# Kernel tuning notes

Measured on AMD Instinct MI355X. Metric: run time of the kernel, lower is better.

## Reference

```python
import jax, jax.numpy as jnp
import numpy as np

B, CIN, HALF, H, W = 4, 3, 32, 512, 512
K_MODE, PAD_MODE, N_LEVELS = 11, 5, 17  # 11x11 mode window, reflect pad 5, round(x*255/16) in 0..16
SLOPE, EPS = 0.01, 1e-5


def _leaky(x):
    return jnp.where(x > 0, x, SLOPE * x)


def _bn(x, g, b):
    # BatchNorm2d in training mode: batch statistics over (B,H,W), biased var
    m = x.mean(axis=(0, 2, 3), keepdims=True)
    v = x.var(axis=(0, 2, 3), keepdims=True)
    return (x - m) * jax.lax.rsqrt(v + EPS) * g[None, :, None, None] + b[None, :, None, None]


def _mode_pool(x):
    # quantize to 17 discrete levels, then sliding-window histogram mode (fused
    # equivalent of unfold + torch.mode; argmax first-hit == smallest tied value)
    k = jnp.clip(jnp.round(x * (255.0 / 16.0)), 0, N_LEVELS - 1).astype(jnp.int32)
    kp = jnp.pad(k, ((0, 0), (0, 0), (PAD_MODE, PAD_MODE), (PAD_MODE, PAD_MODE)), mode='reflect')
    onehot = (kp[..., None] == jnp.arange(N_LEVELS, dtype=jnp.int32)).astype(jnp.float32)
    counts = jax.lax.reduce_window(onehot, 0.0, jax.lax.add,
                                   (1, 1, K_MODE, K_MODE, 1), (1, 1, 1, 1, 1), 'VALID')
    mode_k = jnp.argmax(counts, axis=-1)  # [B,C,H,W]
    return mode_k.astype(jnp.float32) * (16.0 / 256.0)


def _nearest(x, Ho, Wo):
    # torch interpolate(mode='nearest'): src = floor(dst * in/out)
    hi, wi = x.shape[2], x.shape[3]
    ri = (jnp.arange(Ho) * hi) // Ho
    ci = (jnp.arange(Wo) * wi) // Wo
    return x[:, :, ri][:, :, :, ci]


def _forward(x, w1, b1, w2, b2, bn1_g, bn1_b, w3, b3, bn2_g, bn2_b,
             k_down, k_w, bnw_g, bnw_b, k_h, bnh_g, bnh_b):
    xm = _mode_pool(x)  # [B,CIN,H,W]
    # prepare: 1x1 conv -> LeakyReLU -> 1x1 conv -> BN -> LeakyReLU -> depthwise 1x1 -> BN -> LeakyReLU
    h = _leaky(jnp.einsum('bchw,oc->bohw', xm, w1) + b1[None, :, None, None])
    h = jnp.einsum('bchw,oc->bohw', h, w2) + b2[None, :, None, None]
    h = _leaky(_bn(h, bn1_g, bn1_b))
    h = h * w3[None, :, None, None] + b3[None, :, None, None]  # groups=half 1x1 conv
    h = _leaky(_bn(h, bn2_g, bn2_b))
    Bs, half, Ho, Wo = h.shape
    score = jnp.zeros((Bs, 2 * half, Ho, Wo), jnp.float32)
    d = h
    while min(d.shape[2], d.shape[3]) >= 3:  # static pyramid: 512->171->57->19->7->3->1
        d = jax.lax.conv_general_dilated(d, k_down, (3, 3), ((1, 1), (1, 1)),
                                         dimension_numbers=('NCHW', 'OIHW', 'NCHW'),
                                         feature_group_count=half)
        z = _nearest(d, Ho, Wo)
        wbr = _leaky(_bn(z * k_w[None, :, None, None], bnw_g, bnw_b))  # width branch (SharedConv k=1, no bias)
        hbr = _leaky(_bn(z * k_h[None, :, None, None], bnh_g, bnh_b))  # height branch
        # stack(dim=1).reshape => width channels first, then height channels
        score = score + jnp.concatenate([wbr, hbr], axis=1)
    return score


def setup_inputs():
    key = jax.random.key(0)
    ks = jax.random.split(key, 8)
    x = jax.random.uniform(ks[0], (B, CIN, H, W), dtype=jnp.float32)
    s1, s2 = 1.0 / np.sqrt(CIN), 1.0 / np.sqrt(2 * CIN)
    return {
        'x': x,
        'w1': jax.random.uniform(ks[1], (2 * CIN, CIN), jnp.float32, -s1, s1),
        'b1': jax.random.uniform(ks[2], (2 * CIN,), jnp.float32, -s1, s1),
        'w2': jax.random.uniform(ks[3], (HALF, 2 * CIN), jnp.float32, -s2, s2),
        'b2': jax.random.uniform(ks[4], (HALF,), jnp.float32, -s2, s2),
        'bn1_g': jnp.ones((HALF,), jnp.float32),
        'bn1_b': jnp.zeros((HALF,), jnp.float32),
        'w3': jax.random.uniform(ks[5], (HALF,), jnp.float32, -1.0, 1.0),
        'b3': jax.random.uniform(ks[6], (HALF,), jnp.float32, -1.0, 1.0),
        'bn2_g': jnp.ones((HALF,), jnp.float32),
        'bn2_b': jnp.zeros((HALF,), jnp.float32),
        'k_down': jnp.full((HALF, 1, 3, 3), 0.5, jnp.float32),  # SharedConv init
        'k_w': jnp.full((HALF,), 0.5, jnp.float32),
        'bnw_g': jnp.ones((HALF,), jnp.float32),
        'bnw_b': jnp.zeros((HALF,), jnp.float32),
        'k_h': jnp.full((HALF,), 0.5, jnp.float32),
        'bnh_g': jnp.ones((HALF,), jnp.float32),
        'bnh_b': jnp.zeros((HALF,), jnp.float32),
    }


def reference(x, w1, b1, w2, b2, bn1_g, bn1_b, w3, b3, bn2_g, bn2_b,
              k_down, k_w, bnw_g, bnw_b, k_h, bnh_g, bnh_b):
    return _forward(x, w1, b1, w2, b2, bn1_g, bn1_b, w3, b3, bn2_g, bn2_b,
                    k_down, k_w, bnw_g, bnw_b, k_h, bnh_g, bnh_b)
```

## Files before the change

### kernel.cpp

```cpp
#include <hip/hip_runtime.h>

#define HH 512
#define WW 512
#define HW 262144
#define NPIX 1048576
#define NPIXF 1048576.0f

typedef float f4 __attribute__((ext_vector_type(4)));

__device__ __forceinline__ float leaky(float v) { return v > 0.f ? v : 0.01f * v; }

__device__ __forceinline__ float repw(int i, int s) {
    return (float)(((i + 1) * 512 + s - 1) / s - (i * 512 + s - 1) / s);
}

__device__ __forceinline__ void hins7(unsigned long long& h0, unsigned long long& h1,
                                      int val) {
    int lo = val < 9;
    unsigned long long inc = 1ull << ((val * 7 + (lo ? 0 : 1)) & 63);
    h0 += lo ? inc : 0ull;
    h1 += lo ? 0ull : inc;
}
__device__ __forceinline__ void hrem7(unsigned long long& h0, unsigned long long& h1,
                                      int val) {
    int lo = val < 9;
    unsigned long long inc = 1ull << ((val * 7 + (lo ? 0 : 1)) & 63);
    h0 -= lo ? inc : 0ull;
    h1 -= lo ? 0ull : inc;
}

__global__ __launch_bounds__(256) void mode_kernel(const float* __restrict__ x,
                                                   unsigned char* __restrict__ modeq) {
    __shared__ unsigned char q[26 * 272];
    __shared__ __align__(16) unsigned ch[2][267 * 4];
    const int plane = blockIdx.z;
    const int tc0 = blockIdx.x * 256;
    const int tr0 = blockIdx.y * 16;
    const float* xp = x + (size_t)plane * HW;
    for (int idx = threadIdx.x; idx < 26 * 266; idx += 256) {
        int r = idx / 266;
        int cc = idx - r * 266;
        int gr = tr0 + r - 5; gr = gr < 0 ? -gr : (gr > 511 ? 1022 - gr : gr);
        int gc = tc0 + cc - 5; gc = gc < 0 ? -gc : (gc > 511 ? 1022 - gc : gc);
        float v = rintf(xp[gr * WW + gc] * 15.9375f);
        v = fminf(fmaxf(v, 0.f), 16.f);
        q[r * 272 + cc] = (unsigned char)(int)v;
    }
    const int t = threadIdx.x;
    unsigned long long A0 = 0, A1 = 0;
    unsigned long long B0 = 0, B1 = 0;
    __syncthreads();
    for (int r = 0; r < 16; ++r) {
        if (r == 0) {
            #pragma unroll
            for (int v = 0; v < 11; ++v) {
                hins7(A0, A1, q[v * 272 + t]);
                if (t < 10) hins7(B0, B1, q[v * 272 + 256 + t]);
            }
        } else {
            hrem7(A0, A1, q[(r - 1) * 272 + t]);
            hins7(A0, A1, q[(r + 10) * 272 + t]);
            if (t < 10) {
                hrem7(B0, B1, q[(r - 1) * 272 + 256 + t]);
                hins7(B0, B1, q[(r + 10) * 272 + 256 + t]);
            }
        }
        unsigned* cb = ch[r & 1];
        cb[t * 4 + 0] = (unsigned)A0;
        cb[t * 4 + 1] = (unsigned)(A0 >> 32);
        cb[t * 4 + 2] = (unsigned)A1;
        cb[t * 4 + 3] = (unsigned)(A1 >> 32);
        if (t < 10) {
            cb[(256 + t) * 4 + 0] = (unsigned)B0;
            cb[(256 + t) * 4 + 1] = (unsigned)(B0 >> 32);
            cb[(256 + t) * 4 + 2] = (unsigned)B1;
            cb[(256 + t) * 4 + 3] = (unsigned)(B1 >> 32);
        }
        __syncthreads();
        unsigned long long H0 = 0, H1 = 0;
        #pragma unroll
        for (int v = 0; v < 11; ++v) {
            const unsigned* p = &cb[(t + v) * 4];
            H0 += (unsigned long long)p[0] | ((unsigned long long)p[1] << 32);
            H1 += (unsigned long long)p[2] | ((unsigned long long)p[3] << 32);
        }
        unsigned m = 0;
        #pragma unroll
        for (int i = 0; i < 9; ++i) {
            unsigned cnt = (unsigned)(H0 >> (7 * i)) & 0x7Fu;
            unsigned val = (cnt << 8) | (unsigned)(16 - i);
            m = m > val ? m : val;
        }
        #pragma unroll
        for (int i = 9; i < 17; ++i) {
            unsigned cnt = (unsigned)(H1 >> (7 * (i - 9))) & 0x7Fu;
            unsigned val = (cnt << 8) | (unsigned)(16 - i);
            m = m > val ? m : val;
        }
        int k = 16 - (int)(m & 0xFFu);
        modeq[(size_t)plane * HW + (size_t)(tr0 + r) * WW + tc0 + t] = (unsigned char)k;
    }
}

__global__ __launch_bounds__(256) void hist_kernel(const unsigned char* __restrict__ modeq,
                                                   const float* __restrict__ w1,
                                                   const float* __restrict__ b1,
                                                   unsigned* __restrict__ partial,
                                                   float* __restrict__ mpart) {
    __shared__ unsigned lh[4913];
    __shared__ float mred[27][4];
    for (int i = threadIdx.x; i < 4913; i += 256) lh[i] = 0;
    __syncthreads();
    int base = blockIdx.x * 8192;
    int b = base >> 18;
    int hw0 = base & (HW - 1);
    const unsigned char* mp = modeq + (size_t)b * 3 * HW;
    #pragma unroll
    for (int j = 0; j < 8; ++j) {
        int g = threadIdx.x + 256 * j;
        int hw = hw0 + g * 4;
        unsigned u0 = *(const unsigned*)(mp + hw);
        unsigned u1 = *(const unsigned*)(mp + hw + HW);
        unsigned u2 = *(const unsigned*)(mp + hw + 2 * HW);
        #pragma unroll
        for (int k = 0; k < 4; ++k) {
            int k0 = (u0 >> (8 * k)) & 0xFF;
            int k1 = (u1 >> (8 * k)) & 0xFF;
            int k2 = (u2 >> (8 * k)) & 0xFF;
            atomicAdd(&lh[k0 + 17 * k1 + 289 * k2], 1u);
        }
    }
    __syncthreads();
    unsigned* pp = partial + blockIdx.x * 4913;
    for (int i = threadIdx.x; i < 4913; i += 256) pp[i] = lh[i];
    float w1r[18], b1r[6];
    #pragma unroll
    for (int k = 0; k < 18; ++k) w1r[k] = w1[k];
    #pragma unroll
    for (int o = 0; o < 6; ++o) b1r[o] = b1[o];
    float M[27];
    #pragma unroll
    for (int i = 0; i < 27; ++i) M[i] = 0.f;
    for (int bin = threadIdx.x; bin < 4913; bin += 256) {
        float cnt = (float)lh[bin];
        int k0 = bin % 17;
        int r = bin / 17;
        int k1 = r % 17;
        int k2 = r / 17;
        float xm0 = k0 * 0.0625f, xm1 = k1 * 0.0625f, xm2 = k2 * 0.0625f;
        float t1[6];
        #pragma unroll
        for (int o = 0; o < 6; ++o)
            t1[o] = leaky(xm0 * w1r[o * 3] + xm1 * w1r[o * 3 + 1] + xm2 * w1r[o * 3 + 2] + b1r[o]);
        #pragma unroll
        for (int o = 0; o < 6; ++o) M[o] += cnt * t1[o];
        int ii = 6;
        #pragma unroll
        for (int j = 0; j < 6; ++j)
            #pragma unroll
            for (int k = j; k < 6; ++k) { M[ii] += cnt * t1[j] * t1[k]; ++ii; }
    }
    int wv = threadIdx.x >> 6;
    #pragma unroll
    for (int i = 0; i < 27; ++i) {
        float v = M[i];
        #pragma unroll
        for (int off = 32; off >= 1; off >>= 1) v += __shfl_xor(v, off);
        if ((threadIdx.x & 63) == 0) mred[i][wv] = v;
    }
    __syncthreads();
    if (threadIdx.x < 27)
        mpart[blockIdx.x * 27 + threadIdx.x] =
            mred[threadIdx.x][0] + mred[threadIdx.x][1] +
            mred[threadIdx.x][2] + mred[threadIdx.x][3];
}

__global__ __launch_bounds__(256) void redA_kernel(const unsigned* __restrict__ partial,
                                                   float* __restrict__ histf,
                                                   const float* __restrict__ mpart,
                                                   const float* __restrict__ w2,
                                                   const float* __restrict__ b2,
                                                   const float* __restrict__ g1,
                                                   const float* __restrict__ bb1,
                                                   float* __restrict__ p1) {
    if (blockIdx.x < 20) {
        int bin = blockIdx.x * 256 + threadIdx.x;
        if (bin >= 4913) return;
        unsigned s = 0;
        for (int blk = 0; blk < 128; ++blk) s += partial[blk * 4913 + bin];
        histf[bin] = (float)s;
        return;
    }
    __shared__ float mom[27];
    int t = threadIdx.x;
    if (t < 27) {
        float s = 0.f;
        for (int blk = 0; blk < 128; ++blk) s += mpart[blk * 27 + t];
        mom[t] = s;
    }
    __syncthreads();
    if (t < 32) {
        float w2r[6];
        #pragma unroll
        for (int k = 0; k < 6; ++k) w2r[k] = w2[t * 6 + k];
        float b2c = b2[t];
        float wm1 = 0.f;
        #pragma unroll
        for (int k = 0; k < 6; ++k) wm1 += w2r[k] * mom[k];
        float q = 0.f;
        int ii = 6;
        #pragma unroll
        for (int j = 0; j < 6; ++j)
            #pragma unroll
            for (int k = j; k < 6; ++k) {
                float f = w2r[j] * w2r[k] * mom[ii];
                q += (j == k) ? f : 2.f * f;
                ++ii;
            }
        float mean = b2c + wm1 / NPIXF;
        float ex2 = b2c * b2c + 2.f * b2c * (wm1 / NPIXF) + q / NPIXF;
        float var = ex2 - mean * mean;
        float a = g1[t] * rsqrtf(var + 1e-5f);
        p1[t] = a;
        p1[32 + t] = bb1[t] - mean * a;
    }
}

__global__ __launch_bounds__(256) void solveB2_kernel(const float* __restrict__ histf,
                                                      const float* __restrict__ w1,
                                                      const float* __restrict__ b1,
                                                      const float* __restrict__ w2,
                                                      const float* __restrict__ b2,
                                                      const float* __restrict__ p1,
                                                      const float* __restrict__ w3,
                                                      const float* __restrict__ b3,
                                                      const float* __restrict__ g,
                                                      const float* __restrict__ bb,
                                                      float* __restrict__ p2) {
    __shared__ float rs[4], rq[4];
    int c = blockIdx.x;
    float w1r[18], b1r[6], w2r[6];
    #pragma unroll
    for (int k = 0; k < 18; ++k) w1r[k] = w1[k];
    #pragma unroll
    for (int o = 0; o < 6; ++o) b1r[o] = b1[o];
    #pragma unroll
    for (int k = 0; k < 6; ++k) w2r[k] = w2[c * 6 + k];
    float b2c = b2[c];
    float a1 = p1[c], c1 = p1[32 + c];
    float sm = 0.f, sq = 0.f;
    for (int bin = threadIdx.x; bin < 4913; bin += 256) {
        float cnt = histf[bin];
        int k0 = bin % 17;
        int r = bin / 17;
        int k1 = r % 17;
        int k2 = r / 17;
        float xm0 = k0 * 0.0625f, xm1 = k1 * 0.0625f, xm2 = k2 * 0.0625f;
        float t1[6];
        #pragma unroll
        for (int o = 0; o < 6; ++o)
            t1[o] = leaky(xm0 * w1r[o * 3] + xm1 * w1r[o * 3 + 1] + xm2 * w1r[o * 3 + 2] + b1r[o]);
        float h2 = b2c;
        #pragma unroll
        for (int k = 0; k < 6; ++k) h2 += w2r[k] * t1[k];
        float tt = leaky(a1 * h2 + c1);
        sm += cnt * tt;
        sq += cnt * tt * tt;
    }
    #pragma unroll
    for (int off = 32; off >= 1; off >>= 1) {
        sm += __shfl_xor(sm, off);
        sq += __shfl_xor(sq, off);
    }
    if ((threadIdx.x & 63) == 0) { rs[threadIdx.x >> 6] = sm; rq[threadIdx.x >> 6] = sq; }
    __syncthreads();
    if (threadIdx.x == 0) {
        float s = rs[0] + rs[1] + rs[2] + rs[3];
        float qq = rq[0] + rq[1] + rq[2] + rq[3];
        float mt = s / NPIXF;
        float vt = qq / NPIXF - mt * mt;
        float m2 = w3[c] * mt + b3[c];
        float v2 = w3[c] * w3[c] * vt;
        float a = g[c] * rsqrtf(v2 + 1e-5f);
        p2[c] = a;
        p2[32 + c] = bb[c] - m2 * a;
    }
}

__global__ __launch_bounds__(64) void d1_kernel(const unsigned char* __restrict__ modeq,
                                                const float* __restrict__ w1,
                                                const float* __restrict__ b1,
                                                const float* __restrict__ w2,
                                                const float* __restrict__ b2,
                                                const float* __restrict__ w3,
                                                const float* __restrict__ b3,
                                                const float* __restrict__ p1,
                                                const float* __restrict__ p2,
                                                const float* __restrict__ kd,
                                                float* __restrict__ d1) {
    int j = blockIdx.x * 64 + threadIdx.x;
    if (j >= 171) return;
    int i = blockIdx.y;
    int b = blockIdx.z;
    float acc[32];
    #pragma unroll
    for (int c = 0; c < 32; ++c) acc[c] = 0.f;
    const unsigned char* mp = modeq + (size_t)b * 3 * HW;
    #pragma unroll
    for (int u = 0; u < 3; ++u) {
        int r = 3 * i - 1 + u;
        if (r < 0 || r > 511) continue;
        #pragma unroll
        for (int v = 0; v < 3; ++v) {
            int col = 3 * j - 1 + v;
            if (col < 0 || col > 511) continue;
            int off = r * WW + col;
            float xm0 = mp[off] * 0.0625f, xm1 = mp[off + HW] * 0.0625f, xm2 = mp[off + 2 * HW] * 0.0625f;
            float t1[6];
            #pragma unroll
            for (int o = 0; o < 6; ++o)
                t1[o] = leaky(xm0 * w1[o * 3] + xm1 * w1[o * 3 + 1] + xm2 * w1[o * 3 + 2] + b1[o]);
            #pragma unroll
            for (int c = 0; c < 32; ++c) {
                float h2 = b2[c];
                #pragma unroll
                for (int k = 0; k < 6; ++k) h2 += w2[c * 6 + k] * t1[k];
                float t = leaky(h2 * p1[c] + p1[32 + c]);
                float uu = t * w3[c] + b3[c];
                float hv = leaky(uu * p2[c] + p2[32 + c]);
                acc[c] += hv * kd[c * 9 + u * 3 + v];
            }
        }
    }
    size_t base = ((size_t)(b * 32) * 171 + i) * 171 + j;
    #pragma unroll
    for (int c = 0; c < 32; ++c) d1[base + (size_t)c * 29241] = acc[c];
}

__device__ __forceinline__ void red_store(float sm, float sq, float* rsc, float* ps) {
    #pragma unroll
    for (int off = 32; off >= 1; off >>= 1) {
        sm += __shfl_xor(sm, off);
        sq += __shfl_xor(sq, off);
    }
    __syncthreads();
    int wv = threadIdx.x >> 6;
    if ((threadIdx.x & 63) == 0) { rsc[wv] = sm; rsc[8 + wv] = sq; }
    __syncthreads();
    if (threadIdx.x == 0) {
        ps[0] = rsc[0] + rsc[1] + rsc[2] + rsc[3];
        ps[1] = rsc[8] + rsc[9] + rsc[10] + rsc[11];
    }
}

__device__ __forceinline__ void lvl(const float* src, int sin, float* dstL,
                                    float* dstG, int sout, const float* kreg,
                                    float* rsc, float* ps) {
    float sm = 0.f, sq = 0.f;
    int n = sout * sout;
    for (int i = threadIdx.x; i < n; i += 256) {
        int oi = i / sout, oj = i - oi * sout;
        float acc = 0.f;
        #pragma unroll
        for (int u = 0; u < 3; ++u) {
            int r = 3 * oi - 1 + u;
            if ((unsigned)r >= (unsigned)sin) continue;
            #pragma unroll
            for (int v = 0; v < 3; ++v) {
                int cc = 3 * oj - 1 + v;
                if ((unsigned)cc >= (unsigned)sin) continue;
                acc += src[r * sin + cc] * kreg[u * 3 + v];
            }
        }
        dstG[i] = acc;
        if (dstL) dstL[i] = acc;
        float w = repw(oi, sout) * repw(oj, sout);
        sm += w * acc;
        sq += w * acc * acc;
    }
    red_store(sm, sq, rsc, ps);
}

__global__ __launch_bounds__(256) void pyramid_kernel(const float* __restrict__ d1,
                                                      float* __restrict__ d2,
                                                      float* __restrict__ d3,
                                                      float* __restrict__ d4,
                                                      float* __restrict__ d5,
                                                      float* __restrict__ d6,
                                                      const float* __restrict__ kd,
                                                      float* __restrict__ pstats) {
    __shared__ float buf2[3249];
    __shared__ float buf3[361];
    __shared__ float buf4[49];
    __shared__ float buf5[9];
    __shared__ float rsc[16];
    int bc = blockIdx.x;
    int c = bc & 31;
    float kreg[9];
    #pragma unroll
    for (int qq = 0; qq < 9; ++qq) kreg[qq] = kd[c * 9 + qq];
    float* ps = pstats + (size_t)bc * 12;
    const float* s1 = d1 + (size_t)bc * 29241;
    float sm = 0.f, sq = 0.f;
    for (int i = threadIdx.x; i < 29241; i += 256) {
        int oi = i / 171, oj = i - oi * 171;
        float w = repw(oi, 171) * repw(oj, 171);
        float v = s1[i];
        sm += w * v;
        sq += w * v * v;
    }
    red_store(sm, sq, rsc, ps + 0);
    lvl(s1, 171, buf2, d2 + (size_t)bc * 3249, 57, kreg, rsc, ps + 2);
    lvl(buf2, 57, buf3, d3 + (size_t)bc * 361, 19, kreg, rsc, ps + 4);
    lvl(buf3, 19, buf4, d4 + (size_t)bc * 49, 7, kreg, rsc, ps + 6);
    lvl(buf4, 7, buf5, d5 + (size_t)bc * 9, 3, kreg, rsc, ps + 8);
    lvl(buf5, 3, nullptr, d6 + bc, 1, kreg, rsc, ps + 10);
}

__global__ void fin3_kernel(const float* __restrict__ pstats, const float* __restrict__ kw,
                            const float* __restrict__ gw, const float* __restrict__ bw,
                            const float* __restrict__ kh, const float* __restrict__ gh,
                            const float* __restrict__ bh, float* __restrict__ lp) {
    int t = threadIdx.x;
    if (t >= 192) return;
    int l = t >> 5, c = t & 31;
    float sm = 0.f, sq = 0.f;
    #pragma unroll
    for (int b = 0; b < 4; ++b) {
        const float* ps = pstats + (size_t)(b * 32 + c) * 12 + 2 * l;
        sm += ps[0];
        sq += ps[1];
    }
    float mz = sm / NPIXF;
    float vz = sq / NPIXF - mz * mz;
    float kwc = kw[c];
    float aw = gw[c] * rsqrtf(kwc * kwc * vz + 1e-5f);
    float khc = kh[c];
    float ah = gh[c] * rsqrtf(khc * khc * vz + 1e-5f);
    float* o = lp + (size_t)(l * 32 + c) * 4;
    o[0] = kwc * aw;
    o[1] = bw[c] - kwc * mz * aw;
    o[2] = khc * ah;
    o[3] = bh[c] - khc * mz * ah;
}

__global__ __launch_bounds__(256) void final_kernel(const float* __restrict__ d1,
                                                    const float* __restrict__ d2,
                                                    const float* __restrict__ d3,
                                                    const float* __restrict__ d4,
                                                    const float* __restrict__ d5,
                                                    const float* __restrict__ d6,
                                                    const float* __restrict__ lp,
                                                    float* __restrict__ out) {
    const float* ds[6] = {d1, d2, d3, d4, d5, d6};
    const int ss[6] = {171, 57, 19, 7, 3, 1};
    int idx = blockIdx.x * 256 + threadIdx.x;
    #pragma unroll 1
    for (int it = 0; it < 16; ++it, idx += 524288) {
        int w4 = (idx & 127) << 2;
        int h = (idx >> 7) & 511;
        int c = (idx >> 16) & 31;
        int b = idx >> 21;
        float accw[4] = {0.f, 0.f, 0.f, 0.f};
        float acch[4] = {0.f, 0.f, 0.f, 0.f};
        #pragma unroll
        for (int l = 0; l < 6; ++l) {
            int s = ss[l];
            int sh = (h * s) >> 9;
            const float* base = ds[l] + ((size_t)(b * 32 + c) * s + sh) * s;
            const float* a = lp + (size_t)(l * 32 + c) * 4;
            float a0 = a[0], a1 = a[1], a2 = a[2], a3 = a[3];
            #pragma unroll
            for (int k = 0; k < 4; ++k) {
                int sw = ((w4 + k) * s) >> 9;
                float val = base[sw];
                accw[k] += leaky(val * a0 + a1);
                acch[k] += leaky(val * a2 + a3);
            }
        }
        size_t o = (((size_t)(b * 64 + c)) << 18) + ((size_t)h << 9) + w4;
        f4 vw = {accw[0], accw[1], accw[2], accw[3]};
        f4 vh = {acch[0], acch[1], acch[2], acch[3]};
        __builtin_nontemporal_store(vw, (f4*)(out + o));
        __builtin_nontemporal_store(vh, (f4*)(out + o + (((size_t)32) << 18)));
    }
}

extern "C" void kernel_launch(void* const* d_in, const int* in_sizes, int n_in,
                              void* d_out, int out_size, void* d_ws, size_t ws_size,
                              hipStream_t stream) {
    const float* x     = (const float*)d_in[0];
    const float* w1    = (const float*)d_in[1];
    const float* b1    = (const float*)d_in[2];
    const float* w2    = (const float*)d_in[3];
    const float* b2    = (const float*)d_in[4];
    const float* bn1g  = (const float*)d_in[5];
    const float* bn1b  = (const float*)d_in[6];
    const float* w3    = (const float*)d_in[7];
    const float* b3    = (const float*)d_in[8];
    const float* bn2g  = (const float*)d_in[9];
    const float* bn2b  = (const float*)d_in[10];
    const float* kd    = (const float*)d_in[11];
    const float* kw    = (const float*)d_in[12];
    const float* bnwg  = (const float*)d_in[13];
    const float* bnwb  = (const float*)d_in[14];
    const float* kh    = (const float*)d_in[15];
    const float* bnhg  = (const float*)d_in[16];
    const float* bnhb  = (const float*)d_in[17];
    float* out = (float*)d_out;

    char* ws = (char*)d_ws;
    unsigned char* modeq = (unsigned char*)ws;
    float* mpart  = (float*)(ws + 3145728);
    float* pstats = (float*)(ws + 3145728 + 13824);
    float* p1 = (float*)(ws + 3165696);
    float* p2 = p1 + 64;
    float* lp = p2 + 64;
    float* histf = (float*)(ws + 3169280);
    unsigned* partial = (unsigned*)(ws + 3169280 + 20480);
    float* d1 = (float*)(ws + 3189760 + 2515456);
    float* d2 = d1 + 3742848;
    float* d3 = d2 + 415872;
    float* d4 = d3 + 46208;
    float* d5 = d4 + 6272;
    float* d6 = d5 + 1152;

    mode_kernel<<<dim3(2, 32, 12), 256, 0, stream>>>(x, modeq);
    hist_kernel<<<128, 256, 0, stream>>>(modeq, w1, b1, partial, mpart);
    redA_kernel<<<21, 256, 0, stream>>>(partial, histf, mpart, w2, b2, bn1g, bn1b, p1);
    solveB2_kernel<<<32, 256, 0, stream>>>(histf, w1, b1, w2, b2, p1,
                                           w3, b3, bn2g, bn2b, p2);
    d1_kernel<<<dim3(3, 171, 4), 64, 0, stream>>>(modeq, w1, b1, w2, b2, w3, b3,
                                                  p1, p2, kd, d1);
    pyramid_kernel<<<128, 256, 0, stream>>>(d1, d2, d3, d4, d5, d6, kd, pstats);
    fin3_kernel<<<1, 192, 0, stream>>>(pstats, kw, bnwg, bnwb, kh, bnhg, bnhb, lp);
    final_kernel<<<2048, 256, 0, stream>>>(d1, d2, d3, d4, d5, d6, lp, out);
}
```

Baseline: 461.9 us.

## Move BN1 moment computation into per-channel solve kernel and remap final kernel

The 27-moment accumulation moves out of hist_kernel into a combined solveB3 kernel. Each of its 32 channel blocks recomputes the moments from the reduced histogram, caches h2 in shared memory and derives both BN parameter sets, so the redA stage is gone. d1_kernel launches 171x4 blocks of 192 threads instead of 3x171x4 blocks of 64. final_kernel now gives each block a fixed (b,c) and hoists per-level coefficients and column indices out of the row loop. The moment work is repeated 32 times, though on a small histogram.

```diff
diff --git a/kernel.cpp b/kernel.cpp
--- a/kernel.cpp
+++ b/kernel.cpp
@@ -103,12 +103,8 @@
 }
 
 __global__ __launch_bounds__(256) void hist_kernel(const unsigned char* __restrict__ modeq,
-                                                   const float* __restrict__ w1,
-                                                   const float* __restrict__ b1,
-                                                   unsigned* __restrict__ partial,
-                                                   float* __restrict__ mpart) {
+                                                   unsigned* __restrict__ partial) {
     __shared__ unsigned lh[4913];
-    __shared__ float mred[27][4];
     for (int i = threadIdx.x; i < 4913; i += 256) lh[i] = 0;
     __syncthreads();
     int base = blockIdx.x * 8192;
@@ -133,110 +129,32 @@
     __syncthreads();
     unsigned* pp = partial + blockIdx.x * 4913;
     for (int i = threadIdx.x; i < 4913; i += 256) pp[i] = lh[i];
-    float w1r[18], b1r[6];
-    #pragma unroll
-    for (int k = 0; k < 18; ++k) w1r[k] = w1[k];
-    #pragma unroll
-    for (int o = 0; o < 6; ++o) b1r[o] = b1[o];
-    float M[27];
-    #pragma unroll
-    for (int i = 0; i < 27; ++i) M[i] = 0.f;
-    for (int bin = threadIdx.x; bin < 4913; bin += 256) {
-        float cnt = (float)lh[bin];
-        int k0 = bin % 17;
-        int r = bin / 17;
-        int k1 = r % 17;
-        int k2 = r / 17;
-        float xm0 = k0 * 0.0625f, xm1 = k1 * 0.0625f, xm2 = k2 * 0.0625f;
-        float t1[6];
-        #pragma unroll
-        for (int o = 0; o < 6; ++o)
-            t1[o] = leaky(xm0 * w1r[o * 3] + xm1 * w1r[o * 3 + 1] + xm2 * w1r[o * 3 + 2] + b1r[o]);
-        #pragma unroll
-        for (int o = 0; o < 6; ++o) M[o] += cnt * t1[o];
-        int ii = 6;
-        #pragma unroll
-        for (int j = 0; j < 6; ++j)
-            #pragma unroll
-            for (int k = j; k < 6; ++k) { M[ii] += cnt * t1[j] * t1[k]; ++ii; }
-    }
-    int wv = threadIdx.x >> 6;
-    #pragma unroll
-    for (int i = 0; i < 27; ++i) {
-        float v = M[i];
-        #pragma unroll
-        for (int off = 32; off >= 1; off >>= 1) v += __shfl_xor(v, off);
-        if ((threadIdx.x & 63) == 0) mred[i][wv] = v;
-    }
-    __syncthreads();
-    if (threadIdx.x < 27)
-        mpart[blockIdx.x * 27 + threadIdx.x] =
-            mred[threadIdx.x][0] + mred[threadIdx.x][1] +
-            mred[threadIdx.x][2] + mred[threadIdx.x][3];
-}
-
-__global__ __launch_bounds__(256) void redA_kernel(const unsigned* __restrict__ partial,
-                                                   float* __restrict__ histf,
-                                                   const float* __restrict__ mpart,
-                                                   const float* __restrict__ w2,
-                                                   const float* __restrict__ b2,
-                                                   const float* __restrict__ g1,
-                                                   const float* __restrict__ bb1,
-                                                   float* __restrict__ p1) {
-    if (blockIdx.x < 20) {
-        int bin = blockIdx.x * 256 + threadIdx.x;
-        if (bin >= 4913) return;
-        unsigned s = 0;
-        for (int blk = 0; blk < 128; ++blk) s += partial[blk * 4913 + bin];
-        histf[bin] = (float)s;
-        return;
-    }
-    __shared__ float mom[27];
-    int t = threadIdx.x;
-    if (t < 27) {
-        float s = 0.f;
-        for (int blk = 0; blk < 128; ++blk) s += mpart[blk * 27 + t];
-        mom[t] = s;
-    }
-    __syncthreads();
-    if (t < 32) {
-        float w2r[6];
-        #pragma unroll
-        for (int k = 0; k < 6; ++k) w2r[k] = w2[t * 6 + k];
-        float b2c = b2[t];
-        float wm1 = 0.f;
-        #pragma unroll
-        for (int k = 0; k < 6; ++k) wm1 += w2r[k] * mom[k];
-        float q = 0.f;
-        int ii = 6;
-        #pragma unroll
-        for (int j = 0; j < 6; ++j)
-            #pragma unroll
-            for (int k = j; k < 6; ++k) {
-                float f = w2r[j] * w2r[k] * mom[ii];
-                q += (j == k) ? f : 2.f * f;
-                ++ii;
-            }
-        float mean = b2c + wm1 / NPIXF;
-        float ex2 = b2c * b2c + 2.f * b2c * (wm1 / NPIXF) + q / NPIXF;
-        float var = ex2 - mean * mean;
-        float a = g1[t] * rsqrtf(var + 1e-5f);
-        p1[t] = a;
-        p1[32 + t] = bb1[t] - mean * a;
-    }
-}
-
-__global__ __launch_bounds__(256) void solveB2_kernel(const float* __restrict__ histf,
+}
+
+__global__ __launch_bounds__(256) void redhist_kernel(const unsigned* __restrict__ partial,
+                                                      float* __restrict__ histf) {
+    int bin = blockIdx.x * 256 + threadIdx.x;
+    if (bin >= 4913) return;
+    unsigned s = 0;
+    for (int blk = 0; blk < 128; ++blk) s += partial[blk * 4913 + bin];
+    histf[bin] = (float)s;
+}
+
+__global__ __launch_bounds__(256) void solveB3_kernel(const float* __restrict__ histf,
                                                       const float* __restrict__ w1,
                                                       const float* __restrict__ b1,
                                                       const float* __restrict__ w2,
                                                       const float* __restrict__ b2,
-                                                      const float* __restrict__ p1,
+                                                      const float* __restrict__ g1,
+                                                      const float* __restrict__ bb1,
                                                       const float* __restrict__ w3,
                                                       const float* __restrict__ b3,
-                                                      const float* __restrict__ g,
-                                                      const float* __restrict__ bb,
+                                                      const float* __restrict__ g2,
+                                                      const float* __restrict__ bb2,
+                                                      float* __restrict__ p1,
                                                       float* __restrict__ p2) {
+    __shared__ float h2s[4913];
+    __shared__ float red[27][4];
     __shared__ float rs[4], rq[4];
     int c = blockIdx.x;
     float w1r[18], b1r[6], w2r[6];
@@ -247,8 +165,9 @@
     #pragma unroll
     for (int k = 0; k < 6; ++k) w2r[k] = w2[c * 6 + k];
     float b2c = b2[c];
-    float a1 = p1[c], c1 = p1[32 + c];
-    float sm = 0.f, sq = 0.f;
+    float M[27];
+    #pragma unroll
+    for (int i = 0; i < 27; ++i) M[i] = 0.f;
     for (int bin = threadIdx.x; bin < 4913; bin += 256) {
         float cnt = histf[bin];
         int k0 = bin % 17;
@@ -263,7 +182,49 @@
         float h2 = b2c;
         #pragma unroll
         for (int k = 0; k < 6; ++k) h2 += w2r[k] * t1[k];
-        float tt = leaky(a1 * h2 + c1);
+        h2s[bin] = h2;
+        #pragma unroll
+        for (int o = 0; o < 6; ++o) M[o] += cnt * t1[o];
+        int ii = 6;
+        #pragma unroll
+        for (int j = 0; j < 6; ++j)
+            #pragma unroll
+            for (int k = j; k < 6; ++k) { M[ii] += cnt * t1[j] * t1[k]; ++ii; }
+    }
+    int wv = threadIdx.x >> 6;
+    #pragma unroll
+    for (int i = 0; i < 27; ++i) {
+        float v = M[i];
+        #pragma unroll
+        for (int off = 32; off >= 1; off >>= 1) v += __shfl_xor(v, off);
+        if ((threadIdx.x & 63) == 0) red[i][wv] = v;
+    }
+    __syncthreads();
+    float wm1 = 0.f;
+    #pragma unroll
+    for (int k = 0; k < 6; ++k)
+        wm1 += w2r[k] * (red[k][0] + red[k][1] + red[k][2] + red[k][3]);
+    float qd = 0.f;
+    int ii = 6;
+    #pragma unroll
+    for (int j = 0; j < 6; ++j)
+        #pragma unroll
+        for (int k = j; k < 6; ++k) {
+            float mom = red[ii][0] + red[ii][1] + red[ii][2] + red[ii][3];
+            float f = w2r[j] * w2r[k] * mom;
+            qd += (j == k) ? f : 2.f * f;
+            ++ii;
+        }
+    float mean = b2c + wm1 / NPIXF;
+    float ex2 = b2c * b2c + 2.f * b2c * (wm1 / NPIXF) + qd / NPIXF;
+    float var = ex2 - mean * mean;
+    float a1 = g1[c] * rsqrtf(var + 1e-5f);
+    float c1 = bb1[c] - mean * a1;
+    if (threadIdx.x == 0) { p1[c] = a1; p1[32 + c] = c1; }
+    float sm = 0.f, sq = 0.f;
+    for (int bin = threadIdx.x; bin < 4913; bin += 256) {
+        float cnt = histf[bin];
+        float tt = leaky(a1 * h2s[bin] + c1);
         sm += cnt * tt;
         sq += cnt * tt * tt;
     }
@@ -272,7 +233,7 @@
         sm += __shfl_xor(sm, off);
         sq += __shfl_xor(sq, off);
     }
-    if ((threadIdx.x & 63) == 0) { rs[threadIdx.x >> 6] = sm; rq[threadIdx.x >> 6] = sq; }
+    if ((threadIdx.x & 63) == 0) { rs[wv] = sm; rq[wv] = sq; }
     __syncthreads();
     if (threadIdx.x == 0) {
         float s = rs[0] + rs[1] + rs[2] + rs[3];
@@ -281,27 +242,27 @@
         float vt = qq / NPIXF - mt * mt;
         float m2 = w3[c] * mt + b3[c];
         float v2 = w3[c] * w3[c] * vt;
-        float a = g[c] * rsqrtf(v2 + 1e-5f);
+        float a = g2[c] * rsqrtf(v2 + 1e-5f);
         p2[c] = a;
-        p2[32 + c] = bb[c] - m2 * a;
-    }
-}
-
-__global__ __launch_bounds__(64) void d1_kernel(const unsigned char* __restrict__ modeq,
-                                                const float* __restrict__ w1,
-                                                const float* __restrict__ b1,
-                                                const float* __restrict__ w2,
-                                                const float* __restrict__ b2,
-                                                const float* __restrict__ w3,
-                                                const float* __restrict__ b3,
-                                                const float* __restrict__ p1,
-                                                const float* __restrict__ p2,
-                                                const float* __restrict__ kd,
-                                                float* __restrict__ d1) {
-    int j = blockIdx.x * 64 + threadIdx.x;
+        p2[32 + c] = bb2[c] - m2 * a;
+    }
+}
+
+__global__ __launch_bounds__(192) void d1_kernel(const unsigned char* __restrict__ modeq,
+                                                 const float* __restrict__ w1,
+                                                 const float* __restrict__ b1,
+                                                 const float* __restrict__ w2,
+                                                 const float* __restrict__ b2,
+                                                 const float* __restrict__ w3,
+                                                 const float* __restrict__ b3,
+                                                 const float* __restrict__ p1,
+                                                 const float* __restrict__ p2,
+                                                 const float* __restrict__ kd,
+                                                 float* __restrict__ d1) {
+    int j = threadIdx.x;
     if (j >= 171) return;
-    int i = blockIdx.y;
-    int b = blockIdx.z;
+    int i = blockIdx.x;
+    int b = blockIdx.y;
     float acc[32];
     #pragma unroll
     for (int c = 0; c < 32; ++c) acc[c] = 0.f;
@@ -454,31 +415,43 @@
                                                     float* __restrict__ out) {
     const float* ds[6] = {d1, d2, d3, d4, d5, d6};
     const int ss[6] = {171, 57, 19, 7, 3, 1};
-    int idx = blockIdx.x * 256 + threadIdx.x;
+    int bc = blockIdx.x >> 4;
+    int b = bc >> 5, c = bc & 31;
+    int sub = blockIdx.x & 15;
+    int w4 = (threadIdx.x & 127) << 2;
+    int tOff = threadIdx.x >> 7;
+    float ca0[6], ca1[6], ca2[6], ca3[6];
+    int sw[6][4];
+    const float* bases[6];
+    #pragma unroll
+    for (int l = 0; l < 6; ++l) {
+        int s = ss[l];
+        const float* a = lp + (size_t)(l * 32 + c) * 4;
+        ca0[l] = a[0]; ca1[l] = a[1]; ca2[l] = a[2]; ca3[l] = a[3];
+        #pragma unroll
+        for (int k = 0; k < 4; ++k) sw[l][k] = ((w4 + k) * s) >> 9;
+        bases[l] = ds[l] + (size_t)(b * 32 + c) * s * s;
+    }
+    size_t obase = (((size_t)(b * 64 + c)) << 18) + w4;
     #pragma unroll 1
-    for (int it = 0; it < 16; ++it, idx += 524288) {
-        int w4 = (idx & 127) << 2;
-        int h = (idx >> 7) & 511;
-        int c = (idx >> 16) & 31;
-        int b = idx >> 21;
+    for (int it = 0; it < 16; ++it) {
+        int h = sub * 32 + it * 2 + tOff;
         float accw[4] = {0.f, 0.f, 0.f, 0.f};
         float acch[4] = {0.f, 0.f, 0.f, 0.f};
         #pragma unroll
         for (int l = 0; l < 6; ++l) {
             int s = ss[l];
             int sh = (h * s) >> 9;
-            const float* base = ds[l] + ((size_t)(b * 32 + c) * s + sh) * s;
-            const float* a = lp + (size_t)(l * 32 + c) * 4;
-            float a0 = a[0], a1 = a[1], a2 = a[2], a3 = a[3];
+            const float* base = bases[l] + sh * s;
+            float a0 = ca0[l], a1 = ca1[l], a2 = ca2[l], a3 = ca3[l];
             #pragma unroll
             for (int k = 0; k < 4; ++k) {
-                int sw = ((w4 + k) * s) >> 9;
-                float val = base[sw];
+                float val = base[sw[l][k]];
                 accw[k] += leaky(val * a0 + a1);
                 acch[k] += leaky(val * a2 + a3);
             }
         }
-        size_t o = (((size_t)(b * 64 + c)) << 18) + ((size_t)h << 9) + w4;
+        size_t o = obase + ((size_t)h << 9);
         f4 vw = {accw[0], accw[1], accw[2], accw[3]};
         f4 vh = {acch[0], acch[1], acch[2], acch[3]};
         __builtin_nontemporal_store(vw, (f4*)(out + o));
@@ -511,14 +484,13 @@
 
     char* ws = (char*)d_ws;
     unsigned char* modeq = (unsigned char*)ws;
-    float* mpart  = (float*)(ws + 3145728);
-    float* pstats = (float*)(ws + 3145728 + 13824);
-    float* p1 = (float*)(ws + 3165696);
+    float* pstats = (float*)(ws + 3145728);
+    float* p1 = (float*)(ws + 3151872);
     float* p2 = p1 + 64;
     float* lp = p2 + 64;
-    float* histf = (float*)(ws + 3169280);
-    unsigned* partial = (unsigned*)(ws + 3169280 + 20480);
-    float* d1 = (float*)(ws + 3189760 + 2515456);
+    float* histf = (float*)(ws + 3155968);
+    unsigned* partial = (unsigned*)(ws + 3155968 + 20480);
+    float* d1 = (float*)(ws + 3176448 + 2515456);
     float* d2 = d1 + 3742848;
     float* d3 = d2 + 415872;
     float* d4 = d3 + 46208;
@@ -526,12 +498,12 @@
     float* d6 = d5 + 1152;
 
     mode_kernel<<<dim3(2, 32, 12), 256, 0, stream>>>(x, modeq);
-    hist_kernel<<<128, 256, 0, stream>>>(modeq, w1, b1, partial, mpart);
-    redA_kernel<<<21, 256, 0, stream>>>(partial, histf, mpart, w2, b2, bn1g, bn1b, p1);
-    solveB2_kernel<<<32, 256, 0, stream>>>(histf, w1, b1, w2, b2, p1,
-                                           w3, b3, bn2g, bn2b, p2);
-    d1_kernel<<<dim3(3, 171, 4), 64, 0, stream>>>(modeq, w1, b1, w2, b2, w3, b3,
-                                                  p1, p2, kd, d1);
+    hist_kernel<<<128, 256, 0, stream>>>(modeq, partial);
+    redhist_kernel<<<20, 256, 0, stream>>>(partial, histf);
+    solveB3_kernel<<<32, 256, 0, stream>>>(histf, w1, b1, w2, b2, bn1g, bn1b,
+                                           w3, b3, bn2g, bn2b, p1, p2);
+    d1_kernel<<<dim3(171, 4), 192, 0, stream>>>(modeq, w1, b1, w2, b2, w3, b3,
+                                                p1, p2, kd, d1);
     pyramid_kernel<<<128, 256, 0, stream>>>(d1, d2, d3, d4, d5, d6, kd, pstats);
     fin3_kernel<<<1, 192, 0, stream>>>(pstats, kw, bnwg, bnwb, kh, bnhg, bnhb, lp);
     final_kernel<<<2048, 256, 0, stream>>>(d1, d2, d3, d4, d5, d6, lp, out);
```

New measurement: 444.8 us (median of 2 runs). -3.7%, faster.
